# Optimization experiments

Measured on AMD Instinct MI355X. Metric: run time of the kernel, lower is better.

## Reference

```python
import jax, jax.numpy as jnp
import numpy as np

B, N, IN_DIM, HID, OUT_DIM = 16, 1024, 128, 256, 1024
N_LAYERS, SCT_ORDER, GCN_ORDER = 2, 3, 1
TAU, N_ITER, NOISE_SCALE, TANH_SCALE = 0.1, 20, 0.05, 40.0


def _xavier(key, shape):
    # torch xavier_uniform_ on Linear weight [out, in]
    bound = np.sqrt(6.0 / (shape[-1] + shape[-2]))
    return jax.random.uniform(key, shape, jnp.float32, -bound, bound)


def setup_inputs() -> dict:
    key = jax.random.key(0)
    ks = jax.random.split(key, 12)
    L, H = N_LAYERS, HID
    return {
        "X": jax.random.normal(ks[0], (B, N, IN_DIM), jnp.float32),
        "adj": jax.random.uniform(ks[1], (B, N, N), jnp.float32),
        "w_in": _xavier(ks[2], (H, IN_DIM)),
        "b_in": jnp.zeros((H,), jnp.float32),
        "conv_w1": _xavier(ks[3], (L, H, H)),
        "conv_b1": jnp.zeros((L, H), jnp.float32),
        "conv_w2": _xavier(ks[4], (L, H, H)),
        "conv_b2": jnp.zeros((L, H), jnp.float32),
        "conv_a": 0.1 * jax.random.normal(ks[5], (L, 2 * H, 1), jnp.float32),
        "mlp1_w": _xavier(ks[6], (H, H * (1 + L))),
        "mlp1_b": jnp.zeros((H,), jnp.float32),
        "mlp2_w": _xavier(ks[7], (OUT_DIM, H)),
        "mlp2_b": jnp.zeros((OUT_DIM,), jnp.float32),
    }


def leaky(x):
    return jax.nn.leaky_relu(x, 0.01)


def gcn_diffusion(adj, order, X):
    eye = jnp.eye(adj.shape[-1], dtype=adj.dtype)
    A = adj + eye
    dis = A.sum(-1) ** -0.5                      # [B,N]
    A_hat = dis[..., :, None] * A * dis[..., None, :]
    outs, h = [], X
    for _ in range(order):
        h = A_hat @ h
        outs.append(h)
    return outs


def scattering_diffusion(adj, X, order):
    # lazy random walk P = (I + D^{-1} A)/2; wavelets psi_k = P^{2^{k-1}} - P^{2^k}
    Pmat = adj / adj.sum(-1, keepdims=True)

    def applyP(h):
        return 0.5 * (h + Pmat @ h)

    outs = []
    prev = X
    cur = applyP(X)
    outs.append(prev - cur)
    for k in range(2, order + 1):
        nxt = cur
        for _ in range(2 ** (k - 2)):
            nxt = applyP(nxt)
        outs.append(cur - nxt)
        cur = nxt
    return outs


def sct_conv(X, adj, w1, b1, w2, b2, a, moment=1):
    gcn_list = [leaky(g) for g in gcn_diffusion(adj, GCN_ORDER, X)]
    sct_list = [jnp.abs(h) ** moment for h in scattering_diffusion(adj, X, SCT_ORDER)]
    h_all = jnp.stack(gcn_list + sct_list, axis=1)                    # [B,C,N,H]
    x_rep = jnp.broadcast_to(X[:, None], h_all.shape)                 # [B,C,N,H]
    a_in = jnp.concatenate([x_rep, h_all], axis=-1)                   # [B,C,N,2H]
    e = (jax.nn.relu(a_in) @ a)[..., 0]                               # [B,C,N]
    attention = jax.nn.softmax(e + 1e-10, axis=1)[..., None]          # [B,C,N,1]
    h_prime = (attention * h_all).mean(axis=1)                        # [B,N,H]
    h = leaky(h_prime @ w1.T + b1)
    return leaky(h @ w2.T + b2)


def gumbel_sinkhorn(log_alpha, key):
    u = jax.random.uniform(key, log_alpha.shape, log_alpha.dtype)
    noise = -jnp.log(-jnp.log(u + 1e-20) + 1e-20) * NOISE_SCALE
    Z0 = (log_alpha + noise) / TAU

    def step(Z, _):
        Z = Z - jax.scipy.special.logsumexp(Z, axis=-1, keepdims=True)
        Z = Z - jax.scipy.special.logsumexp(Z, axis=-2, keepdims=True)
        return Z, None

    Z, _ = jax.lax.scan(step, Z0, None, length=N_ITER)
    P = jnp.exp(Z)
    P = P / P.sum(-1, keepdims=True)
    P = P / P.sum(-2, keepdims=True)
    return P, Z0


def reference(X, adj, w_in, b_in, conv_w1, conv_b1, conv_w2, conv_b2, conv_a,
              mlp1_w, mlp1_b, mlp2_w, mlp2_b):
    h = X @ w_in.T + b_in                                             # [B,N,H]
    hidden = [h]
    for l in range(N_LAYERS):
        h = sct_conv(h, adj, conv_w1[l], conv_b1[l], conv_w2[l], conv_b2[l], conv_a[l])
        hidden.append(h)
    h = jnp.concatenate(hidden, axis=-1)                              # [B,N,H*(1+L)]
    h = leaky(h @ mlp1_w.T + mlp1_b)
    logits = jnp.tanh(h @ mlp2_w.T + mlp2_b) * TANH_SCALE             # [B,N,N]
    P, gsinit = gumbel_sinkhorn(logits, jax.random.key(42))
    return P, gsinit
```

## Files before the change

kernel.cpp:

```cpp
#include <hip/hip_runtime.h>
#include <cstdint>
#include <cstddef>

#define BB 16
#define NN 1024
#define HD 256
#define IND 128
#define OUTD 1024
#define MROWS (BB*NN)

#define LEAKY(x) ((x) >= 0.0f ? (x) : 0.01f*(x))

typedef short short8 __attribute__((ext_vector_type(8)));
typedef float f32x4 __attribute__((ext_vector_type(4)));

#define GLL16(gsrc, ldst) __builtin_amdgcn_global_load_lds( \
    (const __attribute__((address_space(1))) unsigned int*)(gsrc), \
    (__attribute__((address_space(3))) unsigned int*)(ldst), 16, 0, 0)

#define CFENCE() asm volatile("" ::: "memory")

__device__ inline float wave_sum(float v){
  #pragma unroll
  for (int off=32; off; off>>=1) v += __shfl_xor(v, off, 64);
  return v;
}
__device__ inline float wave_max(float v){
  #pragma unroll
  for (int off=32; off; off>>=1) v = fmaxf(v, __shfl_xor(v, off, 64));
  return v;
}

__device__ inline unsigned short f2bf(float x){
  unsigned u = __float_as_uint(x);
  unsigned r = (u + 0x7fffu + ((u >> 16) & 1u)) >> 16;
  return (unsigned short)r;
}
__device__ inline float bf2f(unsigned short h){
  return __uint_as_float((unsigned)h << 16);
}

__device__ inline float gumbel_noise(unsigned m){
  const unsigned k0 = 0u, k1 = 42u;
  const unsigned ks2 = k0 ^ k1 ^ 0x1BD11BDAu;
  unsigned x0 = 0u, x1 = m;
  x0 += k0; x1 += k1;
  #define TF_ROUND(r) { x0 += x1; x1 = (x1 << (r)) | (x1 >> (32-(r))); x1 ^= x0; }
  TF_ROUND(13) TF_ROUND(15) TF_ROUND(26) TF_ROUND(6)
  x0 += k1;  x1 += ks2 + 1u;
  TF_ROUND(17) TF_ROUND(29) TF_ROUND(16) TF_ROUND(24)
  x0 += ks2; x1 += k0 + 2u;
  TF_ROUND(13) TF_ROUND(15) TF_ROUND(26) TF_ROUND(6)
  x0 += k0;  x1 += k1 + 3u;
  TF_ROUND(17) TF_ROUND(29) TF_ROUND(16) TF_ROUND(24)
  x0 += k1;  x1 += ks2 + 4u;
  TF_ROUND(13) TF_ROUND(15) TF_ROUND(26) TF_ROUND(6)
  x0 += ks2; x1 += k0 + 5u;
  #undef TF_ROUND
  unsigned bits = x0 ^ x1;
  float u = __uint_as_float((bits >> 9) | 0x3f800000u) - 1.0f;
  float t = -__logf(u + 1e-20f);
  return -__logf(t + 1e-20f) * 0.05f;
}

__global__ __launch_bounds__(256) void adj_prep_k(const float* __restrict__ adj,
                                                  float* __restrict__ dis,
                                                  float* __restrict__ rinv,
                                                  unsigned short* __restrict__ abf){
  int tid = threadIdx.x, wid = tid >> 6, lane = tid & 63;
  int row = blockIdx.x*4 + wid;
  const float4* rp = (const float4*)(adj + (size_t)row*NN);
  ushort4* op = (ushort4*)(abf + (size_t)row*NN);
  float s = 0.f;
  #pragma unroll
  for (int p=0;p<4;p++){
    float4 v = rp[lane + p*64];
    s += v.x+v.y+v.z+v.w;
    ushort4 o;
    o.x = f2bf(v.x); o.y = f2bf(v.y); o.z = f2bf(v.z); o.w = f2bf(v.w);
    op[lane + p*64] = o;
  }
  s = wave_sum(s);
  if (lane==0){
    dis[row]  = 1.0f/sqrtf(s + 1.0f);
    rinv[row] = 1.0f/s;
  }
}

__global__ __launch_bounds__(256) void split_flat_k(const float* __restrict__ src,
                                                    unsigned short* __restrict__ h,
                                                    unsigned short* __restrict__ l,
                                                    int n4){
  int gid = blockIdx.x*256 + threadIdx.x;
  if (gid >= n4) return;
  float4 v = ((const float4*)src)[gid];
  ushort4 hh, ll;
  hh.x = f2bf(v.x); ll.x = f2bf(v.x - bf2f(hh.x));
  hh.y = f2bf(v.y); ll.y = f2bf(v.y - bf2f(hh.y));
  hh.z = f2bf(v.z); ll.z = f2bf(v.z - bf2f(hh.z));
  hh.w = f2bf(v.w); ll.w = f2bf(v.w - bf2f(hh.w));
  ((ushort4*)h)[gid] = hh;
  ((ushort4*)l)[gid] = ll;
}

__global__ __launch_bounds__(256) void bconv_t_k(const float* __restrict__ in, int ld,
                                                 const float* __restrict__ scale,
                                                 unsigned short* __restrict__ outT){
  __shared__ float tile[64][68];
  int b  = blockIdx.z;
  int i0 = blockIdx.x*64;
  int c0 = blockIdx.y*64;
  const float* inb = in + (size_t)b*NN*ld;
  unsigned short* ob = outT + (size_t)b*HD*NN;
  int tid = threadIdx.x;
  #pragma unroll
  for (int it=0; it<4; it++){
    int f = tid + it*256;
    int r = f >> 4, c4 = (f & 15)*4;
    float4 v = *(const float4*)(inb + (size_t)(i0+r)*ld + c0 + c4);
    float s = scale ? scale[b*NN + i0 + r] : 1.0f;
    tile[r][c4+0]=v.x*s; tile[r][c4+1]=v.y*s; tile[r][c4+2]=v.z*s; tile[r][c4+3]=v.w*s;
  }
  __syncthreads();
  #pragma unroll
  for (int it=0; it<4; it++){
    int f = tid + it*256;
    int cl = f >> 4, r4 = (f & 15)*4;
    ushort4 o;
    o.x = f2bf(tile[r4+0][cl]);
    o.y = f2bf(tile[r4+1][cl]);
    o.z = f2bf(tile[r4+2][cl]);
    o.w = f2bf(tile[r4+3][cl]);
    *(ushort4*)(ob + (size_t)(c0+cl)*NN + i0 + r4) = o;
  }
}

__global__ __launch_bounds__(512) void gemm_nn_mfma_k(const unsigned short* __restrict__ Abf,
                                                      const unsigned short* __restrict__ Btb,
                                                      const float* __restrict__ Bsrc, int ldb,
                                                      const float* __restrict__ rowscale,
                                                      float* __restrict__ out,
                                                      float* __restrict__ out2,
                                                      const float* __restrict__ sub,
                                                      int mode){
  __shared__ unsigned short Als[4][128][32];
  __shared__ unsigned short Bls[4][128][32];
  int b  = blockIdx.z;
  int n0 = blockIdx.x*128;
  int i0 = blockIdx.y*128;
  const unsigned short* Ab = Abf + (size_t)b*NN*NN + (size_t)i0*NN;
  const unsigned short* Bb = Btb + (size_t)b*HD*NN + (size_t)n0*NN;
  int tid = threadIdx.x;
  int wave = tid >> 6, lane = tid & 63;
  int quad = lane >> 4, l16 = lane & 15;
  int wr = (wave >> 2)*64;
  int wc = (wave & 3)*32;

  int r  = tid >> 2;
  int cg = (((tid & 3) ^ ((r >> 1) & 3)) << 3);
  int wbase = (tid >> 6) << 9;
  const unsigned short* gA = Ab + (size_t)r*NN + cg;
  const unsigned short* gB = Bb + (size_t)r*NN + cg;

  auto STAGE = [&](int tt){
    int buf = tt & 3;
    GLL16(gA + tt*32, &Als[buf][0][0] + wbase);
    GLL16(gB + tt*32, &Bls[buf][0][0] + wbase);
  };

  const int NT = NN/32;
  STAGE(0); STAGE(1);

  f32x4 acc[4][2] = {};

  for (int t = 0; t < NT; ++t){
    if (t+2 < NT){
      STAGE(t+2);
      asm volatile("s_waitcnt vmcnt(4)" ::: "memory");
    } else if (t+1 < NT){
      asm volatile("s_waitcnt vmcnt(2)" ::: "memory");
    } else {
      asm volatile("s_waitcnt vmcnt(0)" ::: "memory");
    }
    __builtin_amdgcn_s_barrier();
    CFENCE();
    int buf = t & 3;
    short8 af[4];
    #pragma unroll
    for (int rt=0; rt<4; rt++){
      int R = wr + rt*16 + l16;
      af[rt] = *(const short8*)&Als[buf][R][(quad ^ ((R >> 1) & 3)) << 3];
    }
    __builtin_amdgcn_s_setprio(1);
    #pragma unroll
    for (int ct=0; ct<2; ct++){
      int Rb = wc + ct*16 + l16;
      short8 bfr = *(const short8*)&Bls[buf][Rb][(quad ^ ((Rb >> 1) & 3)) << 3];
      #pragma unroll
      for (int rt=0; rt<4; rt++)
        acc[rt][ct] = __builtin_amdgcn_mfma_f32_16x16x32_bf16(af[rt], bfr, acc[rt][ct], 0, 0, 0);
    }
    __builtin_amdgcn_s_setprio(0);
  }

  #pragma unroll
  for (int rt=0; rt<4; rt++){
    #pragma unroll
    for (int p=0; p<4; p++){
      int gr = i0 + wr + rt*16 + quad*4 + p;
      int gm = b*NN + gr;
      float sc = rowscale[gm];
      #pragma unroll
      for (int ct=0; ct<2; ct++){
        int gc = n0 + wc + ct*16 + l16;
        float a = acc[rt][ct][p];
        float src = Bsrc[(size_t)gm*ldb + gc];
        float o = (mode == 1) ? 0.5f*(src + sc*a) : LEAKY(sc*(a + sc*src));
        if (out) out[(size_t)gm*HD + gc] = o;
        if (out2){
          float sv = sub ? sub[(size_t)gm*HD + gc] : src;
          out2[(size_t)gm*HD + gc] = fabsf(sv - o);
        }
      }
    }
  }
}

__global__ __launch_bounds__(512) void gemm_nt_mfma_k(const unsigned short* __restrict__ Ah_,
                                                      const unsigned short* __restrict__ Al_,
                                                      int lda,
                                                      const unsigned short* __restrict__ Wh_,
                                                      const unsigned short* __restrict__ Wl_,
                                                      const float* __restrict__ bias,
                                                      float* __restrict__ out, int ldo,
                                                      unsigned short* __restrict__ outh,
                                                      unsigned short* __restrict__ outl,
                                                      int K, int act){
  __shared__ unsigned short Alds[4][128][32];
  __shared__ unsigned short Wlds[4][128][32];
  int o0 = blockIdx.x*128, m0 = blockIdx.y*128;
  int tid = threadIdx.x;
  int wave = tid >> 6, lane = tid & 63;
  int quad = lane >> 4, l16 = lane & 15;
  int wr = (wave >> 2)*64;
  int wc = (wave & 3)*32;

  int r  = tid >> 2;
  int cg = (((tid & 3) ^ ((r >> 1) & 3)) << 3);
  int wbase = (tid >> 6) << 9;
  const unsigned short* gAh = Ah_ + (size_t)(m0 + r)*lda + cg;
  const unsigned short* gAl = Al_ + (size_t)(m0 + r)*lda + cg;
  const unsigned short* gWh = Wh_ + (size_t)(o0 + r)*K + cg;
  const unsigned short* gWl = Wl_ + (size_t)(o0 + r)*K + cg;

  int nk = K >> 5;
  int NT = 3*nk;

  auto STAGE = [&](int tt){
    int buf = tt & 3;
    const unsigned short* sa; const unsigned short* sw; int kc;
    if (tt < nk)        { sa = gAh; sw = gWh; kc = tt << 5; }
    else if (tt < 2*nk) { sa = gAl; sw = gWh; kc = (tt - nk) << 5; }
    else                { sa = gAh; sw = gWl; kc = (tt - 2*nk) << 5; }
    GLL16(sa + kc, &Alds[buf][0][0] + wbase);
    GLL16(sw + kc, &Wlds[buf][0][0] + wbase);
  };

  STAGE(0); STAGE(1);

  f32x4 acc[4][2] = {};

  for (int t = 0; t < NT; ++t){
    if (t+2 < NT){
      STAGE(t+2);
      asm volatile("s_waitcnt vmcnt(4)" ::: "memory");
    } else if (t+1 < NT){
      asm volatile("s_waitcnt vmcnt(2)" ::: "memory");
    } else {
      asm volatile("s_waitcnt vmcnt(0)" ::: "memory");
    }
    __builtin_amdgcn_s_barrier();
    CFENCE();
    int buf = t & 3;
    short8 af[4];
    #pragma unroll
    for (int rt=0; rt<4; rt++){
      int R = wr + rt*16 + l16;
      af[rt] = *(const short8*)&Alds[buf][R][(quad ^ ((R >> 1) & 3)) << 3];
    }
    __builtin_amdgcn_s_setprio(1);
    #pragma unroll
    for (int ct=0; ct<2; ct++){
      int Rb = wc + ct*16 + l16;
      short8 bfr = *(const short8*)&Wlds[buf][Rb][(quad ^ ((Rb >> 1) & 3)) << 3];
      #pragma unroll
      for (int rt=0; rt<4; rt++)
        acc[rt][ct] = __builtin_amdgcn_mfma_f32_16x16x32_bf16(af[rt], bfr, acc[rt][ct], 0, 0, 0);
    }
    __builtin_amdgcn_s_setprio(0);
  }

  #pragma unroll
  for (int rt=0; rt<4; rt++){
    #pragma unroll
    for (int p=0; p<4; p++){
      int gm = m0 + wr + rt*16 + quad*4 + p;
      #pragma unroll
      for (int ct=0; ct<2; ct++){
        int gc = o0 + wc + ct*16 + l16;
        float v = acc[rt][ct][p] + bias[gc];
        if (act == 1){
          v = LEAKY(v);
        } else if (act == 2){
          float vcl = fminf(fmaxf(v, -15.f), 15.f);
          float e = __expf(2.f*vcl);
          float lg = 40.0f * (e - 1.f) / (e + 1.f);
          unsigned flat = (unsigned)gm*1024u + (unsigned)gc;
          v = (lg + gumbel_noise(flat)) / 0.1f;
        }
        if (out) out[(size_t)gm*ldo + gc] = v;
        if (outh){
          unsigned short hh = f2bf(v);
          outh[(size_t)gm*ldo + gc] = hh;
          outl[(size_t)gm*ldo + gc] = f2bf(v - bf2f(hh));
        }
      }
    }
  }
}

__global__ __launch_bounds__(256) void attn_k(const float* __restrict__ c0,
                                              const float* __restrict__ s0,
                                              const float* __restrict__ s1,
                                              const float* __restrict__ s2,
                                              const float* __restrict__ a2,
                                              unsigned short* __restrict__ outh,
                                              unsigned short* __restrict__ outl){
  int tid = threadIdx.x, wid = tid >> 6, lane = tid & 63;
  int row = blockIdx.x*4 + wid;
  size_t base = (size_t)row*HD + lane*4;
  float4 av = *(const float4*)(a2 + lane*4);
  float4 v[4];
  v[0] = *(const float4*)(c0 + base);
  v[1] = *(const float4*)(s0 + base);
  v[2] = *(const float4*)(s1 + base);
  v[3] = *(const float4*)(s2 + base);
  float e[4];
  #pragma unroll
  for (int c=0;c<4;c++){
    float p = fmaxf(v[c].x,0.f)*av.x + fmaxf(v[c].y,0.f)*av.y
            + fmaxf(v[c].z,0.f)*av.z + fmaxf(v[c].w,0.f)*av.w;
    e[c] = wave_sum(p);
  }
  float m = fmaxf(fmaxf(e[0],e[1]), fmaxf(e[2],e[3]));
  float w0 = expf(e[0]-m), w1 = expf(e[1]-m), w2 = expf(e[2]-m), w3 = expf(e[3]-m);
  float inv = 0.25f / (w0+w1+w2+w3);
  float4 o;
  o.x = (w0*v[0].x + w1*v[1].x + w2*v[2].x + w3*v[3].x)*inv;
  o.y = (w0*v[0].y + w1*v[1].y + w2*v[2].y + w3*v[3].y)*inv;
  o.z = (w0*v[0].z + w1*v[1].z + w2*v[2].z + w3*v[3].z)*inv;
  o.w = (w0*v[0].w + w1*v[1].w + w2*v[2].w + w3*v[3].w)*inv;
  ushort4 oh, ol;
  oh.x = f2bf(o.x); ol.x = f2bf(o.x - bf2f(oh.x));
  oh.y = f2bf(o.y); ol.y = f2bf(o.y - bf2f(oh.y));
  oh.z = f2bf(o.z); ol.z = f2bf(o.z - bf2f(oh.z));
  oh.w = f2bf(o.w); ol.w = f2bf(o.w - bf2f(oh.w));
  *(ushort4*)(outh + base) = oh;
  *(ushort4*)(outl + base) = ol;
}

__global__ __launch_bounds__(256) void rowmax_k(const float* __restrict__ Z,
                                                float* __restrict__ alpha){
  int tid = threadIdx.x, wid = tid >> 6, lane = tid & 63;
  int row = blockIdx.x*4 + wid;
  const float4* rp = (const float4*)(Z + (size_t)row*NN);
  float m = -3.4e38f;
  #pragma unroll
  for (int p=0;p<4;p++){
    float4 v = rp[lane + p*64];
    m = fmaxf(m, fmaxf(fmaxf(v.x,v.y), fmaxf(v.z,v.w)));
  }
  m = wave_max(m);
  if (lane==0) alpha[row] = m;
}

__global__ __launch_bounds__(256) void colmax_k(const float* __restrict__ Z,
                                                const float* __restrict__ alpha,
                                                float* __restrict__ pmax){
  int b = blockIdx.y, rc = blockIdx.x;
  int j = threadIdx.x*4;
  const float* Zb = Z + (size_t)b*NN*NN;
  const float* ab = alpha + b*NN;
  float4 m = make_float4(-3.4e38f,-3.4e38f,-3.4e38f,-3.4e38f);
  int r0 = rc*32;
  #pragma unroll 4
  for (int r=r0; r<r0+32; r++){
    float4 v = *(const float4*)(Zb + (size_t)r*NN + j);
    float a = ab[r];
    m.x = fmaxf(m.x, v.x-a); m.y = fmaxf(m.y, v.y-a);
    m.z = fmaxf(m.z, v.z-a); m.w = fmaxf(m.w, v.w-a);
  }
  *(float4*)(pmax + ((size_t)b*32 + rc)*NN + j) = m;
}

__global__ __launch_bounds__(256) void colred_k(const float* __restrict__ pmax,
                                                float* __restrict__ beta){
  int b = blockIdx.y;
  int j = blockIdx.x*256 + threadIdx.x;
  float m = -3.4e38f;
  #pragma unroll
  for (int rc=0; rc<32; rc++)
    m = fmaxf(m, pmax[((size_t)b*32+rc)*NN + j]);
  beta[b*NN + j] = m;
}

__global__ __launch_bounds__(256) void build_e_k(const float* __restrict__ Z,
                                                 const float* __restrict__ alpha,
                                                 const float* __restrict__ beta,
                                                 unsigned short* __restrict__ E,
                                                 unsigned short* __restrict__ Et){
  __shared__ float tile[64][65];
  int b = blockIdx.z;
  int i0 = blockIdx.y*64, j0 = blockIdx.x*64;
  const float* Zb = Z + (size_t)b*NN*NN;
  const float* ab = alpha + b*NN;
  const float* bb = beta  + b*NN;
  unsigned short* Eb  = E  + (size_t)b*NN*NN;
  unsigned short* Etb = Et + (size_t)b*NN*NN;
  int tid = threadIdx.x;
  #pragma unroll
  for (int it=0; it<4; it++){
    int f = tid + it*256;
    int r = f >> 4, c4 = (f & 15)*4;
    float4 v = *(const float4*)(Zb + (size_t)(i0+r)*NN + j0 + c4);
    float a = ab[i0+r];
    float e0 = __expf(v.x - a - bb[j0+c4+0]);
    float e1 = __expf(v.y - a - bb[j0+c4+1]);
    float e2 = __expf(v.z - a - bb[j0+c4+2]);
    float e3 = __expf(v.w - a - bb[j0+c4+3]);
    tile[r][c4+0]=e0; tile[r][c4+1]=e1; tile[r][c4+2]=e2; tile[r][c4+3]=e3;
    ushort4 o; o.x=f2bf(e0); o.y=f2bf(e1); o.z=f2bf(e2); o.w=f2bf(e3);
    *(ushort4*)(Eb + (size_t)(i0+r)*NN + j0 + c4) = o;
  }
  __syncthreads();
  #pragma unroll
  for (int it=0; it<4; it++){
    int f = tid + it*256;
    int r = f >> 4, c4 = (f & 15)*4;
    ushort4 o;
    o.x = f2bf(tile[c4+0][r]);
    o.y = f2bf(tile[c4+1][r]);
    o.z = f2bf(tile[c4+2][r]);
    o.w = f2bf(tile[c4+3][r]);
    *(ushort4*)(Etb + (size_t)(j0+r)*NN + i0 + c4) = o;
  }
}

__global__ __launch_bounds__(256) void mv_k(const unsigned short* __restrict__ M,
                                            const float* __restrict__ v,
                                            float* __restrict__ w, int recip){
  int tid = threadIdx.x, wid = tid >> 6, lane = tid & 63;
  int row = blockIdx.x*4 + wid;
  int b = row >> 10;
  const unsigned short* mp = M + (size_t)row*NN + lane*16;
  float s = 0.f;
  if (v){
    const float* vb = v + b*NN + lane*16;
    #pragma unroll
    for (int h2=0; h2<2; h2++){
      short8 m8 = *(const short8*)(mp + h2*8);
      float4 v0 = *(const float4*)(vb + h2*8);
      float4 v1 = *(const float4*)(vb + h2*8 + 4);
      s += bf2f((unsigned short)m8[0])*v0.x + bf2f((unsigned short)m8[1])*v0.y
         + bf2f((unsigned short)m8[2])*v0.z + bf2f((unsigned short)m8[3])*v0.w
         + bf2f((unsigned short)m8[4])*v1.x + bf2f((unsigned short)m8[5])*v1.y
         + bf2f((unsigned short)m8[6])*v1.z + bf2f((unsigned short)m8[7])*v1.w;
    }
  } else {
    #pragma unroll
    for (int h2=0; h2<2; h2++){
      short8 m8 = *(const short8*)(mp + h2*8);
      #pragma unroll
      for (int q=0;q<8;q++) s += bf2f((unsigned short)m8[q]);
    }
  }
  s = wave_sum(s);
  if (lane==0) w[row] = recip ? 1.0f/s : s;
}

__global__ __launch_bounds__(256) void writep_lin_k(const unsigned short* __restrict__ E,
                                                    const float* __restrict__ ap,
                                                    const float* __restrict__ tp,
                                                    float* __restrict__ P){
  int gid = blockIdx.x*256 + threadIdx.x;
  int row = gid >> 8;
  int j = (gid & 255)*4;
  int b = row >> 10;
  ushort4 e = ((const ushort4*)E)[gid];
  float a = ap[row];
  float4 t = *(const float4*)(tp + (size_t)b*NN + j);
  float4 o;
  o.x = bf2f(e.x)*a/t.x;
  o.y = bf2f(e.y)*a/t.y;
  o.z = bf2f(e.z)*a/t.z;
  o.w = bf2f(e.w)*a/t.w;
  ((float4*)P)[gid] = o;
}

extern "C" void kernel_launch(void* const* d_in, const int* in_sizes, int n_in,
                              void* d_out, int out_size, void* d_ws, size_t ws_size,
                              hipStream_t stream){
  const float* X    = (const float*)d_in[0];
  const float* adj  = (const float*)d_in[1];
  const float* w_in = (const float*)d_in[2];
  const float* b_in = (const float*)d_in[3];
  const float* cw1  = (const float*)d_in[4];
  const float* cb1  = (const float*)d_in[5];
  const float* cw2  = (const float*)d_in[6];
  const float* cb2  = (const float*)d_in[7];
  const float* ca   = (const float*)d_in[8];
  const float* m1w  = (const float*)d_in[9];
  const float* m1b  = (const float*)d_in[10];
  const float* m2w  = (const float*)d_in[11];
  const float* m2b  = (const float*)d_in[12];

  float* outp = (float*)d_out;
  float* Pout = outp;
  float* Z0   = outp + (size_t)16*1024*1024;

  const size_t SLOT = (size_t)4*1024*1024;
  float* s1 = outp + 0*SLOT;
  float* s2 = outp + 1*SLOT;
  float* s3 = outp + 2*SLOT;
  float* s4 = outp + 3*SLOT;
  float* s5 = outp + 4*SLOT;
  unsigned short* adjbf = (unsigned short*)(outp + 6*SLOT);

  unsigned short* Xh  = (unsigned short*)(outp + 0*SLOT);
  unsigned short* Xl  = Xh + (size_t)MROWS*IND;
  unsigned short* s4h = (unsigned short*)(outp + 3*SLOT);
  unsigned short* s4l = s4h + (size_t)MROWS*HD;
  unsigned short* l1h = (unsigned short*)(outp + 0*SLOT);
  unsigned short* l1l = l1h + (size_t)MROWS*HD;
  unsigned short* m1sh = (unsigned short*)(outp + 1*SLOT);
  unsigned short* m1sl = m1sh + (size_t)MROWS*HD;
  unsigned short* Hh = (unsigned short*)(outp + 2*SLOT);
  unsigned short* Hl = Hh + (size_t)MROWS*768;
  float* alpha = s1;
  float* beta  = s1 + 16384;
  float* pmaxb = s1 + 32768;

  float* ws     = (float*)d_ws;
  float* hidden = ws;
  float* dis    = ws + (size_t)12*1024*1024;
  float* rinv   = dis + 16384;
  unsigned short* bt = (unsigned short*)(rinv + 16384);
  unsigned short* wsp = (unsigned short*)(ws + (size_t)15*1024*1024);
  unsigned short* winh = wsp;               unsigned short* winl = winh + 32768;
  unsigned short* w1h  = winl + 32768;      unsigned short* w1l  = w1h + 131072;
  unsigned short* w2h  = w1l + 131072;      unsigned short* w2l  = w2h + 131072;
  unsigned short* m1h  = w2l + 131072;      unsigned short* m1l  = m1h + 196608;
  unsigned short* m2h  = m1l + 196608;      unsigned short* m2l  = m2h + 262144;
  unsigned short* E  = (unsigned short*)ws;
  unsigned short* Et = E + (size_t)MROWS*NN;
  float* av = ws + (size_t)16*1024*1024;
  float* bv = av + 16384;
  float* tv = bv + 16384;

  dim3 blk(256);
  dim3 gEw(4096);
  dim3 gMM(2, 8, 16);
  dim3 gCT(16, 4, 16);

  adj_prep_k<<<gEw, blk, 0, stream>>>(adj, dis, rinv, adjbf);
  split_flat_k<<<dim3(32),  blk, 0, stream>>>(w_in, winh, winl, 8192);
  split_flat_k<<<dim3(128), blk, 0, stream>>>(cw1,  w1h,  w1l,  32768);
  split_flat_k<<<dim3(128), blk, 0, stream>>>(cw2,  w2h,  w2l,  32768);
  split_flat_k<<<dim3(192), blk, 0, stream>>>(m1w,  m1h,  m1l,  49152);
  split_flat_k<<<dim3(256), blk, 0, stream>>>(m2w,  m2h,  m2l,  65536);
  split_flat_k<<<dim3(2048), blk, 0, stream>>>(X, Xh, Xl, 524288);

  gemm_nt_mfma_k<<<dim3(2,128), dim3(512), 0, stream>>>(Xh, Xl, IND,
                                                        winh, winl, b_in,
                                                        hidden, 768, nullptr, nullptr,
                                                        IND, 0);

  for (int l=0; l<2; l++){
    const float* h_in = hidden + l*HD;
    unsigned short* wl1h = w1h + (size_t)l*65536;
    unsigned short* wl1l = w1l + (size_t)l*65536;
    unsigned short* wl2h = w2h + (size_t)l*65536;
    unsigned short* wl2l = w2l + (size_t)l*65536;
    const float* b1 = cb1 + (size_t)l*HD;
    const float* b2 = cb2 + (size_t)l*HD;
    const float* a2 = ca  + (size_t)l*2*HD + HD;

    bconv_t_k<<<gCT, blk, 0, stream>>>(h_in, 768, dis, bt);
    gemm_nn_mfma_k<<<gMM, dim3(512), 0, stream>>>(adjbf, bt, h_in, 768, dis, s2, nullptr, nullptr, 2);
    bconv_t_k<<<gCT, blk, 0, stream>>>(h_in, 768, nullptr, bt);
    gemm_nn_mfma_k<<<gMM, dim3(512), 0, stream>>>(adjbf, bt, h_in, 768, rinv, s1, s3, nullptr, 1);
    bconv_t_k<<<gCT, blk, 0, stream>>>(s1, HD, nullptr, bt);
    gemm_nn_mfma_k<<<gMM, dim3(512), 0, stream>>>(adjbf, bt, s1, HD, rinv, s4, s5, nullptr, 1);
    bconv_t_k<<<gCT, blk, 0, stream>>>(s4, HD, nullptr, bt);
    gemm_nn_mfma_k<<<gMM, dim3(512), 0, stream>>>(adjbf, bt, s4, HD, rinv, s1, nullptr, nullptr, 1);
    bconv_t_k<<<gCT, blk, 0, stream>>>(s1, HD, nullptr, bt);
    gemm_nn_mfma_k<<<gMM, dim3(512), 0, stream>>>(adjbf, bt, s1, HD, rinv, nullptr, s1, s4, 1);
    attn_k<<<gEw, blk, 0, stream>>>(s2, s3, s5, s1, a2, s4h, s4l);
    gemm_nt_mfma_k<<<dim3(2,128), dim3(512), 0, stream>>>(s4h, s4l, HD,
                                                          wl1h, wl1l, b1,
                                                          nullptr, HD, l1h, l1l,
                                                          HD, 1);
    gemm_nt_mfma_k<<<dim3(2,128), dim3(512), 0, stream>>>(l1h, l1l, HD,
                                                          wl2h, wl2l, b2,
                                                          hidden + (l+1)*HD, 768,
                                                          nullptr, nullptr, HD, 1);
  }

  split_flat_k<<<dim3(12288), blk, 0, stream>>>(hidden, Hh, Hl, 3145728);
  gemm_nt_mfma_k<<<dim3(2,128), dim3(512), 0, stream>>>(Hh, Hl, 768,
                                                        m1h, m1l, m1b,
                                                        nullptr, HD, m1sh, m1sl,
                                                        768, 1);
  gemm_nt_mfma_k<<<dim3(8,128), dim3(512), 0, stream>>>(m1sh, m1sl, HD,
                                                        m2h, m2l, m2b,
                                                        Z0, OUTD, nullptr, nullptr,
                                                        HD, 2);

  rowmax_k<<<gEw, blk, 0, stream>>>(Z0, alpha);
  colmax_k<<<dim3(32,16), blk, 0, stream>>>(Z0, alpha, pmaxb);
  colred_k<<<dim3(4,16), blk, 0, stream>>>(pmaxb, beta);
  build_e_k<<<dim3(16,16,16), blk, 0, stream>>>(Z0, alpha, beta, E, Et);

  mv_k<<<gEw, blk, 0, stream>>>(E,  nullptr, av, 1);
  mv_k<<<gEw, blk, 0, stream>>>(Et, av,      bv, 1);
  for (int t=1; t<20; t++){
    mv_k<<<gEw, blk, 0, stream>>>(E,  bv, av, 1);
    mv_k<<<gEw, blk, 0, stream>>>(Et, av, bv, 1);
  }
  mv_k<<<gEw, blk, 0, stream>>>(E,  bv, av, 1);
  mv_k<<<gEw, blk, 0, stream>>>(Et, av, tv, 0);
  writep_lin_k<<<dim3(16384), blk, 0, stream>>>(E, av, tv, Pout);
}
```

Measured before the change: 1.202 ms.

## Store Sinkhorn exp matrix in 8-bit format, restructure GEMM pipelines and tile order

The Sinkhorn exponent matrices E and Et are now stored in a custom 8-bit float encoding (3 mantissa bits) instead of bf16. This halves the bytes read by the repeated matrix-vector passes and by the final P write. The NN GEMM drops from 4-stage to 2-stage LDS double buffering with an extra barrier per step, and both GEMMs remap block indices to group tiles, likely for L2/XCD locality. The split-precision NT GEMM now loads the hi and lo operands together and issues all three MFMAs per k-chunk instead of making three passes. The 8-bit encoding loses precision in the Sinkhorn normalisation and may hurt accuracy.

New measurement: 1.216 ms. Within noise of the previous version (+1.2%).

```diff
diff --git a/kernel.cpp b/kernel.cpp
--- a/kernel.cpp
+++ b/kernel.cpp
@@ -38,6 +38,22 @@
 }
 __device__ inline float bf2f(unsigned short h){
   return __uint_as_float((unsigned)h << 16);
+}
+
+__device__ inline unsigned enc_e(float x){
+  unsigned u = __float_as_uint(x);
+  u += 0xFFFFFu + ((u>>20)&1u);
+  int E = (int)(u>>23) - 112;
+  if (E <= 0){
+    unsigned Ms = (unsigned)__float2int_rn(x * 131072.0f);
+    return (Ms >= 8u) ? 8u : Ms;
+  }
+  return ((unsigned)E<<3) | ((u>>20)&7u);
+}
+__device__ inline float dec_e(unsigned k){
+  unsigned E = k>>3, M = k&7u;
+  float nrm = __uint_as_float(((E+112u)<<23)|(M<<20));
+  return E ? nrm : (float)M * 7.62939453125e-6f;
 }
 
 __device__ inline float gumbel_noise(unsigned m){
@@ -143,11 +159,13 @@
                                                       float* __restrict__ out2,
                                                       const float* __restrict__ sub,
                                                       int mode){
-  __shared__ unsigned short Als[4][128][32];
-  __shared__ unsigned short Bls[4][128][32];
-  int b  = blockIdx.z;
-  int n0 = blockIdx.x*128;
-  int i0 = blockIdx.y*128;
+  __shared__ unsigned short Als[2][128][32];
+  __shared__ unsigned short Bls[2][128][32];
+  int s = blockIdx.x + (blockIdx.y<<1) + (blockIdx.z<<4);
+  int idx = (s&7)*32 + (s>>3);
+  int b  = idx >> 4;
+  int i0 = ((idx>>1)&7)*128;
+  int n0 = (idx&1)*128;
   const unsigned short* Ab = Abf + (size_t)b*NN*NN + (size_t)i0*NN;
   const unsigned short* Bb = Btb + (size_t)b*HD*NN + (size_t)n0*NN;
   int tid = threadIdx.x;
@@ -162,29 +180,27 @@
   const unsigned short* gA = Ab + (size_t)r*NN + cg;
   const unsigned short* gB = Bb + (size_t)r*NN + cg;
 
-  auto STAGE = [&](int tt){
-    int buf = tt & 3;
-    GLL16(gA + tt*32, &Als[buf][0][0] + wbase);
-    GLL16(gB + tt*32, &Bls[buf][0][0] + wbase);
+  auto STAGE = [&](int c){
+    int buf = c & 1;
+    GLL16(gA + (c<<5), &Als[buf][0][0] + wbase);
+    GLL16(gB + (c<<5), &Bls[buf][0][0] + wbase);
   };
 
-  const int NT = NN/32;
-  STAGE(0); STAGE(1);
+  const int NC = NN/32;
+  STAGE(0);
 
   f32x4 acc[4][2] = {};
 
-  for (int t = 0; t < NT; ++t){
-    if (t+2 < NT){
-      STAGE(t+2);
-      asm volatile("s_waitcnt vmcnt(4)" ::: "memory");
-    } else if (t+1 < NT){
+  for (int c = 0; c < NC; ++c){
+    if (c+1 < NC){
+      STAGE(c+1);
       asm volatile("s_waitcnt vmcnt(2)" ::: "memory");
     } else {
       asm volatile("s_waitcnt vmcnt(0)" ::: "memory");
     }
     __builtin_amdgcn_s_barrier();
     CFENCE();
-    int buf = t & 3;
+    int buf = c & 1;
     short8 af[4];
     #pragma unroll
     for (int rt=0; rt<4; rt++){
@@ -201,6 +217,9 @@
         acc[rt][ct] = __builtin_amdgcn_mfma_f32_16x16x32_bf16(af[rt], bfr, acc[rt][ct], 0, 0, 0);
     }
     __builtin_amdgcn_s_setprio(0);
+    CFENCE();
+    __builtin_amdgcn_s_barrier();
+    CFENCE();
   }
 
   #pragma unroll
@@ -236,9 +255,15 @@
                                                       unsigned short* __restrict__ outh,
                                                       unsigned short* __restrict__ outl,
                                                       int K, int act){
-  __shared__ unsigned short Alds[4][128][32];
-  __shared__ unsigned short Wlds[4][128][32];
-  int o0 = blockIdx.x*128, m0 = blockIdx.y*128;
+  __shared__ unsigned short AhL[2][128][32], AlL[2][128][32];
+  __shared__ unsigned short WhL[2][128][32], WlL[2][128][32];
+  int gx = gridDim.x;
+  int sh = (gx == 2) ? 1 : 3;
+  int s = blockIdx.x + blockIdx.y*gx;
+  int nwg = gx*gridDim.y;
+  int idx = (s&7)*(nwg>>3) + (s>>3);
+  int o0 = (idx & (gx-1))*128;
+  int m0 = (idx >> sh)*128;
   int tid = threadIdx.x;
   int wave = tid >> 6, lane = tid & 63;
   int quad = lane >> 4, l16 = lane & 15;
@@ -253,51 +278,56 @@
   const unsigned short* gWh = Wh_ + (size_t)(o0 + r)*K + cg;
   const unsigned short* gWl = Wl_ + (size_t)(o0 + r)*K + cg;
 
-  int nk = K >> 5;
-  int NT = 3*nk;
-
-  auto STAGE = [&](int tt){
-    int buf = tt & 3;
-    const unsigned short* sa; const unsigned short* sw; int kc;
-    if (tt < nk)        { sa = gAh; sw = gWh; kc = tt << 5; }
-    else if (tt < 2*nk) { sa = gAl; sw = gWh; kc = (tt - nk) << 5; }
-    else                { sa = gAh; sw = gWl; kc = (tt - 2*nk) << 5; }
-    GLL16(sa + kc, &Alds[buf][0][0] + wbase);
-    GLL16(sw + kc, &Wlds[buf][0][0] + wbase);
+  int NC = K >> 5;
+
+  auto STAGE = [&](int c){
+    int buf = c & 1; int kc = c << 5;
+    GLL16(gAh + kc, &AhL[buf][0][0] + wbase);
+    GLL16(gAl + kc, &AlL[buf][0][0] + wbase);
+    GLL16(gWh + kc, &WhL[buf][0][0] + wbase);
+    GLL16(gWl + kc, &WlL[buf][0][0] + wbase);
   };
 
-  STAGE(0); STAGE(1);
+  STAGE(0);
 
   f32x4 acc[4][2] = {};
 
-  for (int t = 0; t < NT; ++t){
-    if (t+2 < NT){
-      STAGE(t+2);
+  for (int c = 0; c < NC; ++c){
+    if (c+1 < NC){
+      STAGE(c+1);
       asm volatile("s_waitcnt vmcnt(4)" ::: "memory");
-    } else if (t+1 < NT){
-      asm volatile("s_waitcnt vmcnt(2)" ::: "memory");
     } else {
       asm volatile("s_waitcnt vmcnt(0)" ::: "memory");
     }
     __builtin_amdgcn_s_barrier();
     CFENCE();
-    int buf = t & 3;
-    short8 af[4];
+    int buf = c & 1;
+    short8 ah[4], al[4];
     #pragma unroll
     for (int rt=0; rt<4; rt++){
       int R = wr + rt*16 + l16;
-      af[rt] = *(const short8*)&Alds[buf][R][(quad ^ ((R >> 1) & 3)) << 3];
+      int sc = (quad ^ ((R >> 1) & 3)) << 3;
+      ah[rt] = *(const short8*)&AhL[buf][R][sc];
+      al[rt] = *(const short8*)&AlL[buf][R][sc];
     }
     __builtin_amdgcn_s_setprio(1);
     #pragma unroll
     for (int ct=0; ct<2; ct++){
       int Rb = wc + ct*16 + l16;
-      short8 bfr = *(const short8*)&Wlds[buf][Rb][(quad ^ ((Rb >> 1) & 3)) << 3];
+      int sc = (quad ^ ((Rb >> 1) & 3)) << 3;
+      short8 wh = *(const short8*)&WhL[buf][Rb][sc];
+      short8 wl = *(const short8*)&WlL[buf][Rb][sc];
       #pragma unroll
-      for (int rt=0; rt<4; rt++)
-        acc[rt][ct] = __builtin_amdgcn_mfma_f32_16x16x32_bf16(af[rt], bfr, acc[rt][ct], 0, 0, 0);
+      for (int rt=0; rt<4; rt++){
+        acc[rt][ct] = __builtin_amdgcn_mfma_f32_16x16x32_bf16(ah[rt], wh, acc[rt][ct], 0, 0, 0);
+        acc[rt][ct] = __builtin_amdgcn_mfma_f32_16x16x32_bf16(al[rt], wh, acc[rt][ct], 0, 0, 0);
+        acc[rt][ct] = __builtin_amdgcn_mfma_f32_16x16x32_bf16(ah[rt], wl, acc[rt][ct], 0, 0, 0);
+      }
     }
     __builtin_amdgcn_s_setprio(0);
+    CFENCE();
+    __builtin_amdgcn_s_barrier();
+    CFENCE();
   }
 
   #pragma unroll
@@ -417,16 +447,16 @@
 __global__ __launch_bounds__(256) void build_e_k(const float* __restrict__ Z,
                                                  const float* __restrict__ alpha,
                                                  const float* __restrict__ beta,
-                                                 unsigned short* __restrict__ E,
-                                                 unsigned short* __restrict__ Et){
+                                                 unsigned char* __restrict__ E,
+                                                 unsigned char* __restrict__ Et){
   __shared__ float tile[64][65];
   int b = blockIdx.z;
   int i0 = blockIdx.y*64, j0 = blockIdx.x*64;
   const float* Zb = Z + (size_t)b*NN*NN;
   const float* ab = alpha + b*NN;
   const float* bb = beta  + b*NN;
-  unsigned short* Eb  = E  + (size_t)b*NN*NN;
-  unsigned short* Etb = Et + (size_t)b*NN*NN;
+  unsigned char* Eb  = E  + (size_t)b*NN*NN;
+  unsigned char* Etb = Et + (size_t)b*NN*NN;
   int tid = threadIdx.x;
   #pragma unroll
   for (int it=0; it<4; it++){
@@ -439,56 +469,58 @@
     float e2 = __expf(v.z - a - bb[j0+c4+2]);
     float e3 = __expf(v.w - a - bb[j0+c4+3]);
     tile[r][c4+0]=e0; tile[r][c4+1]=e1; tile[r][c4+2]=e2; tile[r][c4+3]=e3;
-    ushort4 o; o.x=f2bf(e0); o.y=f2bf(e1); o.z=f2bf(e2); o.w=f2bf(e3);
-    *(ushort4*)(Eb + (size_t)(i0+r)*NN + j0 + c4) = o;
+    uchar4 o;
+    o.x=(unsigned char)enc_e(e0); o.y=(unsigned char)enc_e(e1);
+    o.z=(unsigned char)enc_e(e2); o.w=(unsigned char)enc_e(e3);
+    *(uchar4*)(Eb + (size_t)(i0+r)*NN + j0 + c4) = o;
   }
   __syncthreads();
   #pragma unroll
   for (int it=0; it<4; it++){
     int f = tid + it*256;
     int r = f >> 4, c4 = (f & 15)*4;
-    ushort4 o;
-    o.x = f2bf(tile[c4+0][r]);
-    o.y = f2bf(tile[c4+1][r]);
-    o.z = f2bf(tile[c4+2][r]);
-    o.w = f2bf(tile[c4+3][r]);
-    *(ushort4*)(Etb + (size_t)(j0+r)*NN + i0 + c4) = o;
-  }
-}
-
-__global__ __launch_bounds__(256) void mv_k(const unsigned short* __restrict__ M,
+    uchar4 o;
+    o.x = (unsigned char)enc_e(tile[c4+0][r]);
+    o.y = (unsigned char)enc_e(tile[c4+1][r]);
+    o.z = (unsigned char)enc_e(tile[c4+2][r]);
+    o.w = (unsigned char)enc_e(tile[c4+3][r]);
+    *(uchar4*)(Etb + (size_t)(j0+r)*NN + i0 + c4) = o;
+  }
+}
+
+__global__ __launch_bounds__(256) void mv_k(const unsigned char* __restrict__ M,
                                             const float* __restrict__ v,
                                             float* __restrict__ w, int recip){
   int tid = threadIdx.x, wid = tid >> 6, lane = tid & 63;
   int row = blockIdx.x*4 + wid;
   int b = row >> 10;
-  const unsigned short* mp = M + (size_t)row*NN + lane*16;
+  uint4 mw = *((const uint4*)(M + (size_t)row*NN) + lane);
   float s = 0.f;
   if (v){
     const float* vb = v + b*NN + lane*16;
-    #pragma unroll
-    for (int h2=0; h2<2; h2++){
-      short8 m8 = *(const short8*)(mp + h2*8);
-      float4 v0 = *(const float4*)(vb + h2*8);
-      float4 v1 = *(const float4*)(vb + h2*8 + 4);
-      s += bf2f((unsigned short)m8[0])*v0.x + bf2f((unsigned short)m8[1])*v0.y
-         + bf2f((unsigned short)m8[2])*v0.z + bf2f((unsigned short)m8[3])*v0.w
-         + bf2f((unsigned short)m8[4])*v1.x + bf2f((unsigned short)m8[5])*v1.y
-         + bf2f((unsigned short)m8[6])*v1.z + bf2f((unsigned short)m8[7])*v1.w;
-    }
+    float4 v0 = *(const float4*)(vb);
+    float4 v1 = *(const float4*)(vb+4);
+    float4 v2 = *(const float4*)(vb+8);
+    float4 v3 = *(const float4*)(vb+12);
+    s += dec_e(mw.x&255u)*v0.x + dec_e((mw.x>>8)&255u)*v0.y
+       + dec_e((mw.x>>16)&255u)*v0.z + dec_e(mw.x>>24)*v0.w;
+    s += dec_e(mw.y&255u)*v1.x + dec_e((mw.y>>8)&255u)*v1.y
+       + dec_e((mw.y>>16)&255u)*v1.z + dec_e(mw.y>>24)*v1.w;
+    s += dec_e(mw.z&255u)*v2.x + dec_e((mw.z>>8)&255u)*v2.y
+       + dec_e((mw.z>>16)&255u)*v2.z + dec_e(mw.z>>24)*v2.w;
+    s += dec_e(mw.w&255u)*v3.x + dec_e((mw.w>>8)&255u)*v3.y
+       + dec_e((mw.w>>16)&255u)*v3.z + dec_e(mw.w>>24)*v3.w;
   } else {
-    #pragma unroll
-    for (int h2=0; h2<2; h2++){
-      short8 m8 = *(const short8*)(mp + h2*8);
-      #pragma unroll
-      for (int q=0;q<8;q++) s += bf2f((unsigned short)m8[q]);
-    }
+    s += dec_e(mw.x&255u) + dec_e((mw.x>>8)&255u) + dec_e((mw.x>>16)&255u) + dec_e(mw.x>>24);
+    s += dec_e(mw.y&255u) + dec_e((mw.y>>8)&255u) + dec_e((mw.y>>16)&255u) + dec_e(mw.y>>24);
+    s += dec_e(mw.z&255u) + dec_e((mw.z>>8)&255u) + dec_e((mw.z>>16)&255u) + dec_e(mw.z>>24);
+    s += dec_e(mw.w&255u) + dec_e((mw.w>>8)&255u) + dec_e((mw.w>>16)&255u) + dec_e(mw.w>>24);
   }
   s = wave_sum(s);
   if (lane==0) w[row] = recip ? 1.0f/s : s;
 }
 
-__global__ __launch_bounds__(256) void writep_lin_k(const unsigned short* __restrict__ E,
+__global__ __launch_bounds__(256) void writep_lin_k(const unsigned char* __restrict__ E,
                                                     const float* __restrict__ ap,
                                                     const float* __restrict__ tp,
                                                     float* __restrict__ P){
@@ -496,14 +528,14 @@
   int row = gid >> 8;
   int j = (gid & 255)*4;
   int b = row >> 10;
-  ushort4 e = ((const ushort4*)E)[gid];
+  uchar4 e = ((const uchar4*)E)[gid];
   float a = ap[row];
   float4 t = *(const float4*)(tp + (size_t)b*NN + j);
   float4 o;
-  o.x = bf2f(e.x)*a/t.x;
-  o.y = bf2f(e.y)*a/t.y;
-  o.z = bf2f(e.z)*a/t.z;
-  o.w = bf2f(e.w)*a/t.w;
+  o.x = dec_e(e.x)*a/t.x;
+  o.y = dec_e(e.y)*a/t.y;
+  o.z = dec_e(e.z)*a/t.z;
+  o.w = dec_e(e.w)*a/t.w;
   ((float4*)P)[gid] = o;
 }
 
@@ -561,8 +593,8 @@
   unsigned short* w2h  = w1l + 131072;      unsigned short* w2l  = w2h + 131072;
   unsigned short* m1h  = w2l + 131072;      unsigned short* m1l  = m1h + 196608;
   unsigned short* m2h  = m1l + 196608;      unsigned short* m2l  = m2h + 262144;
-  unsigned short* E  = (unsigned short*)ws;
-  unsigned short* Et = E + (size_t)MROWS*NN;
+  unsigned char* E  = (unsigned char*)ws;
+  unsigned char* Et = E + (size_t)MROWS*NN;
   float* av = ws + (size_t)16*1024*1024;
   float* bv = av + 16384;
   float* tv = bv + 16384;
```
